# Performance work log

Hardware: AMD Instinct MI355X
Metric: run time of the kernel (lower is better)

The kernel has to match this reference:

```python
import jax, jax.numpy as jnp
import numpy as np

D_MODEL, H, KV, D = 2048, 32, 8, 64
G = H // KV  # groups = 4
B, T = 1, 2048


def rotate_half(x):
    # interleaved rotation: (-x1, x0, -x3, x2, ...)
    x_even = x[..., ::2]
    x_odd = x[..., 1::2]
    return jnp.stack((-x_odd, x_even), axis=-1).reshape(x.shape)


def setup_inputs() -> dict:
    key = jax.random.key(0)
    kx, kq, kk, kv, ko = jax.random.split(key, 5)
    x = jax.random.normal(kx, (B, T, D_MODEL), dtype=jnp.float32)
    # RoPE frequency table: freqs[0]=cos, freqs[1]=sin, each [T, D] with pairwise-repeated angles
    inv_freq = 1.0 / (10000.0 ** (jnp.arange(0, D, 2, dtype=jnp.float32) / D))  # [D/2]
    angles = jnp.arange(T, dtype=jnp.float32)[:, None] * inv_freq[None, :]       # [T, D/2]
    angles = jnp.repeat(angles, 2, axis=-1)                                       # [T, D]
    freqs = jnp.stack((jnp.cos(angles), jnp.sin(angles)), axis=0)                 # [2, T, D]
    # causal mask, broadcastable to [B, H, T, T]
    mask = jnp.tril(jnp.ones((T, T), dtype=bool))[None, None]
    s = 0.02
    Wq = s * jax.random.normal(kq, (D_MODEL, H * D), dtype=jnp.float32)
    Wk = s * jax.random.normal(kk, (D_MODEL, KV * D), dtype=jnp.float32)
    Wv = s * jax.random.normal(kv, (D_MODEL, KV * D), dtype=jnp.float32)
    Wo = s * jax.random.normal(ko, (D_MODEL, D_MODEL), dtype=jnp.float32)
    return {"x": x, "freqs": freqs, "mask": mask, "Wq": Wq, "Wk": Wk, "Wv": Wv, "Wo": Wo}


def reference(x, freqs, mask, Wq, Wk, Wv, Wo):
    b, t, _ = x.shape
    Q = (x @ Wq).reshape(b, t, H, D)
    K = (x @ Wk).reshape(b, t, KV, D)
    V = (x @ Wv).reshape(b, t, KV, D)
    cos = freqs[0, :t][None, :, None, :]  # [1,T,1,D]
    sin = freqs[1, :t][None, :, None, :]
    Q = Q * cos + rotate_half(Q) * sin
    K = K * cos + rotate_half(K) * sin
    # GQA: repeat each KV head `groups` times along the head axis
    K = jnp.repeat(K, G, axis=2)  # [B,T,H,D]
    V = jnp.repeat(V, G, axis=2)
    scale = D ** -0.5
    scores = jnp.einsum('bqhd,bkhd->bhqk', Q, K) * scale  # [B,H,T,T]
    scores = jnp.where(mask, scores, -jnp.inf)
    attn = jax.nn.softmax(scores, axis=-1)  # dropout=0.0 (eval) -> identity
    out = jnp.einsum('bhqk,bkhd->bqhd', attn, V).reshape(b, t, H * D)
    return out @ Wo
```

## Files before the change

kernel.cpp:

```cpp
#include <hip/hip_runtime.h>
#include <hip/hip_bf16.h>

#define T_SEQ  2048
#define DMODEL 2048
#define NH     32
#define NKV    8
#define HD     64

typedef __attribute__((ext_vector_type(8))) short bf16x8;
typedef __attribute__((ext_vector_type(4))) short bf16x4;
typedef __attribute__((ext_vector_type(4))) float f32x4;

__device__ __forceinline__ unsigned short f2bf(float f) {
    unsigned int u = __float_as_uint(f);
    return (unsigned short)((u + 0x7FFFu + ((u >> 16) & 1u)) >> 16);
}
__device__ __forceinline__ float bf2f(unsigned short b) {
    return __uint_as_float(((unsigned int)b) << 16);
}
__device__ __forceinline__ unsigned int pk2bf(float a, float b) {
    float2 f; f.x = a; f.y = b;
    __hip_bfloat162 h = __float22bfloat162_rn(f);
    union { __hip_bfloat162 h; unsigned int u; } cv; cv.h = h;
    return cv.u;
}
__device__ __forceinline__ int is_bf16(const void* __restrict__ freqs) {
    return ((const unsigned int*)freqs)[0] != 0x3F800000u;
}
__device__ __forceinline__ float ldf(const void* __restrict__ p, size_t i, int bf) {
    return bf ? bf2f(((const unsigned short*)p)[i]) : ((const float*)p)[i];
}

__global__ __launch_bounds__(256) void prep_kernel(const void* __restrict__ x,
                                                   const void* __restrict__ Wq,
                                                   const void* __restrict__ Wk,
                                                   const void* __restrict__ Wv,
                                                   unsigned short* __restrict__ xb,
                                                   unsigned short* __restrict__ WqT,
                                                   unsigned short* __restrict__ WkT,
                                                   unsigned short* __restrict__ WvT,
                                                   const void* __restrict__ freqs) {
    const int bf = is_bf16(freqs);
    const int t  = threadIdx.x;
    const int z  = blockIdx.z;
    if (z == 3) {
        const int r0 = blockIdx.y * 64, c0 = blockIdx.x * 64;
#pragma unroll
        for (int it = 0; it < 16; ++it) {
            int e = t + it * 256;
            size_t idx = (size_t)(r0 + (e >> 6)) * DMODEL + c0 + (e & 63);
            xb[idx] = bf ? ((const unsigned short*)x)[idx] : f2bf(((const float*)x)[idx]);
        }
        return;
    }
    const void* W; unsigned short* Wt; int N;
    if (z == 0)      { W = Wq; Wt = WqT; N = 2048; }
    else if (z == 1) { if (blockIdx.x >= 8) return; W = Wk; Wt = WkT; N = 512; }
    else             { if (blockIdx.x >= 8) return; W = Wv; Wt = WvT; N = 512; }
    __shared__ unsigned short Tl[64][65];
    const int n0 = blockIdx.x * 64, k0 = blockIdx.y * 64;
#pragma unroll
    for (int it = 0; it < 16; ++it) {
        int e = t + it * 256;
        int r = e >> 6, c = e & 63;
        Tl[r][c] = bf ? ((const unsigned short*)W)[(size_t)(k0 + r) * N + n0 + c]
                      : f2bf(((const float*)W)[(size_t)(k0 + r) * N + n0 + c]);
    }
    __syncthreads();
#pragma unroll
    for (int it = 0; it < 16; ++it) {
        int e = t + it * 256;
        int r = e >> 6, c = e & 63;
        Wt[(size_t)(n0 + r) * DMODEL + k0 + c] = Tl[c][r];
    }
}

__global__ __launch_bounds__(256) void trans_one(const void* __restrict__ W,
                                                 unsigned short* __restrict__ Wt,
                                                 const void* __restrict__ freqs) {
    const int bf = is_bf16(freqs);
    __shared__ unsigned short Tl[64][65];
    const int t = threadIdx.x;
    const int n0 = blockIdx.x * 64, k0 = blockIdx.y * 64;
#pragma unroll
    for (int it = 0; it < 16; ++it) {
        int e = t + it * 256;
        int r = e >> 6, c = e & 63;
        Tl[r][c] = bf ? ((const unsigned short*)W)[(size_t)(k0 + r) * DMODEL + n0 + c]
                      : f2bf(((const float*)W)[(size_t)(k0 + r) * DMODEL + n0 + c]);
    }
    __syncthreads();
#pragma unroll
    for (int it = 0; it < 16; ++it) {
        int e = t + it * 256;
        int r = e >> 6, c = e & 63;
        Wt[(size_t)(n0 + r) * DMODEL + k0 + c] = Tl[c][r];
    }
}

template <int WM, int WN, int CMODE>
__global__ __launch_bounds__(256) void gemm_mfma(const unsigned short* __restrict__ A,
                                                 const unsigned short* __restrict__ Bt,
                                                 void* __restrict__ C,
                                                 int M, int N, int K,
                                                 const void* __restrict__ freqs) {
    constexpr int BM  = 32 * WM;
    constexpr int BN  = 32 * WN;
    constexpr int LDT = 40;
    __shared__ unsigned short As[2][BM * LDT];
    __shared__ unsigned short Bs[2][BN * LDT];

    const int t    = threadIdx.x;
    const int w    = t >> 6;
    const int lane = t & 63;
    const int wm   = w & 1, wn = w >> 1;
    const int m0   = wm * WM * 16;
    const int n0   = wn * WN * 16;
    const int lrow = lane & 15;
    const int quad = lane >> 4;
    const int bm   = blockIdx.y * BM;
    const int bn   = blockIdx.x * BN;
    int cbf = 0;
    if (CMODE == 2) cbf = is_bf16(freqs);

    constexpr int AIT = (BM * 4) / 256;
    constexpr int BIT = (BN * 4) / 256;
    bf16x8 apre[AIT], bpre[BIT];

#pragma unroll
    for (int it = 0; it < AIT; ++it) {
        int c = t + it * 256;
        apre[it] = *(const bf16x8*)&A[(size_t)(bm + (c >> 2)) * K + (c & 3) * 8];
    }
#pragma unroll
    for (int it = 0; it < BIT; ++it) {
        int c = t + it * 256;
        bpre[it] = *(const bf16x8*)&Bt[(size_t)(bn + (c >> 2)) * K + (c & 3) * 8];
    }
#pragma unroll
    for (int it = 0; it < AIT; ++it) {
        int c = t + it * 256;
        *(bf16x8*)&As[0][(c >> 2) * LDT + (c & 3) * 8] = apre[it];
    }
#pragma unroll
    for (int it = 0; it < BIT; ++it) {
        int c = t + it * 256;
        *(bf16x8*)&Bs[0][(c >> 2) * LDT + (c & 3) * 8] = bpre[it];
    }

    f32x4 acc[WM][WN];
#pragma unroll
    for (int i = 0; i < WM; ++i)
#pragma unroll
        for (int j = 0; j < WN; ++j) acc[i][j] = (f32x4){0.f, 0.f, 0.f, 0.f};

    const int nk = K >> 5;
    for (int ki = 0; ki < nk; ++ki) {
        __syncthreads();
        const int buf = ki & 1;
        const bool pre = (ki + 1 < nk);
        if (pre) {
            const int k0 = (ki + 1) * 32;
#pragma unroll
            for (int it = 0; it < AIT; ++it) {
                int c = t + it * 256;
                apre[it] = *(const bf16x8*)&A[(size_t)(bm + (c >> 2)) * K + k0 + (c & 3) * 8];
            }
#pragma unroll
            for (int it = 0; it < BIT; ++it) {
                int c = t + it * 256;
                bpre[it] = *(const bf16x8*)&Bt[(size_t)(bn + (c >> 2)) * K + k0 + (c & 3) * 8];
            }
        }

        bf16x8 af[WM], bfr[WN];
#pragma unroll
        for (int i = 0; i < WM; ++i)
            af[i] = *(const bf16x8*)&As[buf][(m0 + i * 16 + lrow) * LDT + quad * 8];
#pragma unroll
        for (int j = 0; j < WN; ++j)
            bfr[j] = *(const bf16x8*)&Bs[buf][(n0 + j * 16 + lrow) * LDT + quad * 8];
#pragma unroll
        for (int i = 0; i < WM; ++i)
#pragma unroll
            for (int j = 0; j < WN; ++j)
                acc[i][j] = __builtin_amdgcn_mfma_f32_16x16x32_bf16(af[i], bfr[j], acc[i][j], 0, 0, 0);

        if (pre) {
#pragma unroll
            for (int it = 0; it < AIT; ++it) {
                int c = t + it * 256;
                *(bf16x8*)&As[buf ^ 1][(c >> 2) * LDT + (c & 3) * 8] = apre[it];
            }
#pragma unroll
            for (int it = 0; it < BIT; ++it) {
                int c = t + it * 256;
                *(bf16x8*)&Bs[buf ^ 1][(c >> 2) * LDT + (c & 3) * 8] = bpre[it];
            }
        }
    }

#pragma unroll
    for (int i = 0; i < WM; ++i)
#pragma unroll
        for (int j = 0; j < WN; ++j)
#pragma unroll
            for (int r = 0; r < 4; ++r) {
                int row = bm + m0 + i * 16 + quad * 4 + r;
                int col = bn + n0 + j * 16 + lrow;
                size_t idx = (size_t)row * N + col;
                float v = acc[i][j][r];
                if (CMODE == 1) ((unsigned short*)C)[idx] = f2bf(v);
                else { if (cbf) ((unsigned short*)C)[idx] = f2bf(v); else ((float*)C)[idx] = v; }
            }
}

__global__ __launch_bounds__(256) void kv_gemm(const unsigned short* __restrict__ A,
                                               const unsigned short* __restrict__ WkT,
                                               const unsigned short* __restrict__ WvT,
                                               unsigned short* __restrict__ Kb,
                                               unsigned short* __restrict__ Vt_g) {
    constexpr int LDT = 40;
    __shared__ unsigned short As[2][64 * LDT];
    __shared__ unsigned short Bs[2][64 * LDT];

    const int zv   = blockIdx.z;
    const unsigned short* Bt = zv ? WvT : WkT;
    const int t    = threadIdx.x;
    const int w    = t >> 6;
    const int lane = t & 63;
    const int wm   = w & 1, wn = w >> 1;
    const int m0   = wm * 32;
    const int n0   = wn * 32;
    const int lrow = lane & 15;
    const int quad = lane >> 4;
    const int bm   = blockIdx.y * 64;
    const int bn   = blockIdx.x * 64;
    const int K    = DMODEL, N = NKV * HD;

    bf16x8 apre, bpre;
    apre = *(const bf16x8*)&A[(size_t)(bm + (t >> 2)) * K + (t & 3) * 8];
    bpre = *(const bf16x8*)&Bt[(size_t)(bn + (t >> 2)) * K + (t & 3) * 8];
    *(bf16x8*)&As[0][(t >> 2) * LDT + (t & 3) * 8] = apre;
    *(bf16x8*)&Bs[0][(t >> 2) * LDT + (t & 3) * 8] = bpre;

    f32x4 acc[2][2];
#pragma unroll
    for (int i = 0; i < 2; ++i)
#pragma unroll
        for (int j = 0; j < 2; ++j) acc[i][j] = (f32x4){0.f, 0.f, 0.f, 0.f};

    const int nk = K >> 5;
    for (int ki = 0; ki < nk; ++ki) {
        __syncthreads();
        const int buf = ki & 1;
        const bool pre = (ki + 1 < nk);
        if (pre) {
            const int k0 = (ki + 1) * 32;
            apre = *(const bf16x8*)&A[(size_t)(bm + (t >> 2)) * K + k0 + (t & 3) * 8];
            bpre = *(const bf16x8*)&Bt[(size_t)(bn + (t >> 2)) * K + k0 + (t & 3) * 8];
        }
        bf16x8 af[2], bfr[2];
#pragma unroll
        for (int i = 0; i < 2; ++i)
            af[i] = *(const bf16x8*)&As[buf][(m0 + i * 16 + lrow) * LDT + quad * 8];
#pragma unroll
        for (int j = 0; j < 2; ++j)
            bfr[j] = *(const bf16x8*)&Bs[buf][(n0 + j * 16 + lrow) * LDT + quad * 8];
#pragma unroll
        for (int i = 0; i < 2; ++i)
#pragma unroll
            for (int j = 0; j < 2; ++j)
                acc[i][j] = __builtin_amdgcn_mfma_f32_16x16x32_bf16(af[i], bfr[j], acc[i][j], 0, 0, 0);
        if (pre) {
            *(bf16x8*)&As[buf ^ 1][(t >> 2) * LDT + (t & 3) * 8] = apre;
            *(bf16x8*)&Bs[buf ^ 1][(t >> 2) * LDT + (t & 3) * 8] = bpre;
        }
    }

#pragma unroll
    for (int i = 0; i < 2; ++i)
#pragma unroll
        for (int j = 0; j < 2; ++j)
#pragma unroll
            for (int r = 0; r < 4; ++r) {
                int row = bm + m0 + i * 16 + quad * 4 + r;
                int col = bn + n0 + j * 16 + lrow;
                unsigned short v = f2bf(acc[i][j][r]);
                if (zv) Vt_g[(size_t)col * T_SEQ + row] = v;
                else    Kb[(size_t)row * N + col] = v;
            }
}

__global__ void rope_kernel(unsigned short* __restrict__ Qb, unsigned short* __restrict__ Kb,
                            const void* __restrict__ freqs) {
    const int bf = is_bf16(freqs);
    int idx = blockIdx.x * blockDim.x + threadIdx.x;
    const int nq = T_SEQ * NH * 32;
    unsigned short* X; int nh; float scale; int li;
    if (idx < nq) { X = Qb; nh = NH; scale = 0.125f; li = idx; }
    else          { X = Kb; nh = NKV; scale = 1.0f; li = idx - nq;
                    if (li >= T_SEQ * NKV * 32) return; }
    int i = li & 31;
    int h = (li >> 5) % nh;
    int t = li / (nh * 32);
    float c = ldf(freqs, (size_t)t * 64 + 2 * i, bf);
    float s = ldf(freqs, (size_t)T_SEQ * 64 + (size_t)t * 64 + 2 * i, bf);
    int base = (t * nh + h) * HD + 2 * i;
    float x0 = bf2f(X[base]), x1 = bf2f(X[base + 1]);
    X[base]     = f2bf((x0 * c - x1 * s) * scale);
    X[base + 1] = f2bf((x1 * c + x0 * s) * scale);
}

__global__ __launch_bounds__(256) void attn_kernel(const unsigned short* __restrict__ Qb,
                                                   const unsigned short* __restrict__ Kb,
                                                   const unsigned short* __restrict__ Vt_g,
                                                   unsigned short* __restrict__ AO,
                                                   unsigned short* __restrict__ arena,
                                                   float* __restrict__ lpart) {
    __shared__ unsigned short Kf[2][8 * 64 * 8];
    __shared__ unsigned short Vf[2][8 * 64 * 8];

    const int t    = threadIdx.x;
    const int w    = t >> 6;
    const int lane = t & 63;
    const int lrow = lane & 15;
    const int quad = lane >> 4;
    const int hp   = blockIdx.y;
    const int kvh  = hp >> 1;
    const int h0   = kvh * 4 + (hp & 1) * 2;
    const int bxr  = 71 - (int)blockIdx.x;

    int qt, j, s;
    if (bxr < 8)       { qt = bxr; j = 0; s = 1; }
    else if (bxr < 24) { qt = 8 + ((bxr - 8) >> 1); j = (bxr - 8) & 1; s = 2; }
    else               { int e = bxr - 24; qt = 16 + e / 3; j = e % 3; s = 3; }
    const int n    = qt + 1;
    const int base = n / s, rem = n % s;
    const int nch  = base + (j < rem ? 1 : 0);
    const int cs   = j * base + (j < rem ? j : rem);
    const int q0   = qt * 64;
    const int koff = cs * 64;
    const bool mask_last = (cs + nch - 1) == qt;

    bf16x8 q_frag[2][2];
#pragma unroll
    for (int hh = 0; hh < 2; ++hh) {
        const unsigned short* qp = Qb + (size_t)(q0 + w * 16 + lrow) * (NH * HD) + (h0 + hh) * HD;
        q_frag[hh][0] = *(const bf16x8*)&qp[quad * 8];
        q_frag[hh][1] = *(const bf16x8*)&qp[32 + quad * 8];
    }

    const int    krow = 16 * w + lrow;
    const size_t vrow = (size_t)(kvh * HD + 16 * w + lrow) * T_SEQ;

    union U8 { bf16x8 v; bf16x4 hh[2]; unsigned short s[8]; unsigned int u32[4]; };

    bf16x8 kpre[2];
    bf16x4 vpre[2][2];
#pragma unroll
    for (int i = 0; i < 2; ++i) {
        kpre[i] = *(const bf16x8*)&Kb[(size_t)(koff + krow) * (NKV * HD) + kvh * HD + i * 32 + quad * 8];
        vpre[i][0] = *(const bf16x4*)&Vt_g[vrow + koff + i * 32 + quad * 4];
        vpre[i][1] = *(const bf16x4*)&Vt_g[vrow + koff + i * 32 + 16 + quad * 4];
    }
#pragma unroll
    for (int i = 0; i < 2; ++i) {
        *(bf16x8*)&Kf[0][((2 * w + i) * 64 + lane) * 8] = kpre[i];
        U8 u; u.hh[0] = vpre[i][0]; u.hh[1] = vpre[i][1];
        *(bf16x8*)&Vf[0][((2 * w + i) * 64 + lane) * 8] = u.v;
    }

    float l_s[2] = {0.0f, 0.0f};
    f32x4 oacc[2][4];
#pragma unroll
    for (int hh = 0; hh < 2; ++hh)
#pragma unroll
        for (int nc = 0; nc < 4; ++nc) oacc[hh][nc] = (f32x4){0.f, 0.f, 0.f, 0.f};

    for (int c = 0; c < nch; ++c) {
        __syncthreads();
        const int buf = c & 1;
        const bool pre = (c + 1 < nch);
        if (pre) {
            const int kb2 = koff + (c + 1) * 64;
#pragma unroll
            for (int i = 0; i < 2; ++i) {
                kpre[i] = *(const bf16x8*)&Kb[(size_t)(kb2 + krow) * (NKV * HD) + kvh * HD + i * 32 + quad * 8];
                vpre[i][0] = *(const bf16x4*)&Vt_g[vrow + kb2 + i * 32 + quad * 4];
                vpre[i][1] = *(const bf16x4*)&Vt_g[vrow + kb2 + i * 32 + 16 + quad * 4];
            }
        }

        f32x4 sacc[2][4];
#pragma unroll
        for (int hh = 0; hh < 2; ++hh)
#pragma unroll
            for (int kc = 0; kc < 4; ++kc) sacc[hh][kc] = (f32x4){0.f, 0.f, 0.f, 0.f};
#pragma unroll
        for (int kh = 0; kh < 2; ++kh) {
#pragma unroll
            for (int kc = 0; kc < 4; ++kc) {
                bf16x8 kf = *(const bf16x8*)&Kf[buf][((kc * 2 + kh) * 64 + lane) * 8];
                sacc[0][kc] = __builtin_amdgcn_mfma_f32_16x16x32_bf16(kf, q_frag[0][kh], sacc[0][kc], 0, 0, 0);
                sacc[1][kc] = __builtin_amdgcn_mfma_f32_16x16x32_bf16(kf, q_frag[1][kh], sacc[1][kc], 0, 0, 0);
            }
        }

        if (c == nch - 1 && mask_last) {
            const int qrow  = q0 + w * 16 + lrow;
            const int kbase = koff + c * 64 + quad * 4;
#pragma unroll
            for (int kc = 0; kc < 4; ++kc)
#pragma unroll
                for (int r = 0; r < 4; ++r)
                    if (kbase + kc * 16 + r > qrow) { sacc[0][kc][r] = -INFINITY; sacc[1][kc][r] = -INFINITY; }
        }

        bf16x8 pf[2][2];
#pragma unroll
        for (int hh = 0; hh < 2; ++hh) {
            float rsum = 0.0f;
#pragma unroll
            for (int kc = 0; kc < 4; ++kc)
#pragma unroll
                for (int r = 0; r < 4; ++r) {
                    sacc[hh][kc][r] = __expf(sacc[hh][kc][r]);
                    rsum += sacc[hh][kc][r];
                }
            l_s[hh] += rsum;
#pragma unroll
            for (int kh = 0; kh < 2; ++kh) {
                U8 u;
                u.u32[0] = pk2bf(sacc[hh][2 * kh][0], sacc[hh][2 * kh][1]);
                u.u32[1] = pk2bf(sacc[hh][2 * kh][2], sacc[hh][2 * kh][3]);
                u.u32[2] = pk2bf(sacc[hh][2 * kh + 1][0], sacc[hh][2 * kh + 1][1]);
                u.u32[3] = pk2bf(sacc[hh][2 * kh + 1][2], sacc[hh][2 * kh + 1][3]);
                pf[hh][kh] = u.v;
            }
        }

#pragma unroll
        for (int kh = 0; kh < 2; ++kh) {
#pragma unroll
            for (int nc = 0; nc < 4; ++nc) {
                bf16x8 vu = *(const bf16x8*)&Vf[buf][((nc * 2 + kh) * 64 + lane) * 8];
                oacc[0][nc] = __builtin_amdgcn_mfma_f32_16x16x32_bf16(pf[0][kh], vu, oacc[0][nc], 0, 0, 0);
                oacc[1][nc] = __builtin_amdgcn_mfma_f32_16x16x32_bf16(pf[1][kh], vu, oacc[1][nc], 0, 0, 0);
            }
        }

        if (pre) {
#pragma unroll
            for (int i = 0; i < 2; ++i) {
                *(bf16x8*)&Kf[buf ^ 1][((2 * w + i) * 64 + lane) * 8] = kpre[i];
                U8 u; u.hh[0] = vpre[i][0]; u.hh[1] = vpre[i][1];
                *(bf16x8*)&Vf[buf ^ 1][((2 * w + i) * 64 + lane) * 8] = u.v;
            }
        }
    }

#pragma unroll
    for (int hh = 0; hh < 2; ++hh) {
        const int h = h0 + hh;
        float ls = l_s[hh];
        ls += __shfl_xor(ls, 16);
        ls += __shfl_xor(ls, 32);

        if (s == 1) {
            const float linv = 1.0f / ls;
            float l_o[4];
#pragma unroll
            for (int r = 0; r < 4; ++r)
                l_o[r] = __shfl(linv, (lane & 48) | (quad * 4 + r));
#pragma unroll
            for (int nc = 0; nc < 4; ++nc)
#pragma unroll
                for (int r = 0; r < 4; ++r) {
                    int row = q0 + w * 16 + quad * 4 + r;
                    AO[(size_t)row * (NH * HD) + h * HD + nc * 16 + lrow] = f2bf(oacc[hh][nc][r] * l_o[r]);
                }
        } else {
            if (quad == 0)
                lpart[(((size_t)h * 32 + qt) * 3 + j) * 64 + (w * 16 + lrow)] = ls;
            if (j == 0) {
#pragma unroll
                for (int nc = 0; nc < 4; ++nc)
#pragma unroll
                    for (int r = 0; r < 4; ++r) {
                        int row = q0 + w * 16 + quad * 4 + r;
                        AO[(size_t)row * (NH * HD) + h * HD + nc * 16 + lrow] = f2bf(oacc[hh][nc][r]);
                    }
            } else {
                const int slot = (qt < 16) ? (qt - 8) : (8 + (qt - 16) * 2 + (j - 1));
                unsigned short* ap = arena + ((size_t)h * 40 + slot) * 4096;
#pragma unroll
                for (int nc = 0; nc < 4; ++nc)
#pragma unroll
                    for (int r = 0; r < 4; ++r)
                        ap[(size_t)(w * 16 + quad * 4 + r) * 64 + nc * 16 + lrow] = f2bf(oacc[hh][nc][r]);
            }
        }
    }
}

__global__ __launch_bounds__(256) void combine_kernel(unsigned short* __restrict__ AO,
                                                      const unsigned short* __restrict__ arena,
                                                      const float* __restrict__ lpart) {
    int idx = blockIdx.x * 256 + threadIdx.x;
    int row1 = idx >> 11;
    int col  = idx & 2047;
    int qt   = 8 + (row1 >> 6);
    int r    = row1 & 63;
    int h    = col >> 6;
    int d    = col & 63;
    int s    = (qt < 16) ? 2 : 3;

    size_t aoidx = (size_t)(512 + row1) * 2048 + col;
    float o = bf2f(AO[aoidx]);
    float l = lpart[(((size_t)h * 32 + qt) * 3 + 0) * 64 + r];
#pragma unroll
    for (int j = 1; j < 3; ++j) {
        if (j >= s) break;
        int slot = (qt < 16) ? (qt - 8) : (8 + (qt - 16) * 2 + (j - 1));
        o += bf2f(arena[((size_t)h * 40 + slot) * 4096 + (size_t)r * 64 + d]);
        l += lpart[(((size_t)h * 32 + qt) * 3 + j) * 64 + r];
    }
    AO[aoidx] = f2bf(o / l);
}

extern "C" void kernel_launch(void* const* d_in, const int* in_sizes, int n_in,
                              void* d_out, int out_size, void* d_ws, size_t ws_size,
                              hipStream_t stream) {
    const void* x     = d_in[0];
    const void* freqs = d_in[1];
    const void* Wq = d_in[3];
    const void* Wk = d_in[4];
    const void* Wv = d_in[5];
    const void* Wo = d_in[6];

    char* ws = (char*)d_ws;
    unsigned short* Qb   = (unsigned short*)(ws);
    unsigned short* Kb   = (unsigned short*)(ws + (8u  << 20));
    unsigned short* Vt_g = (unsigned short*)(ws + (10u << 20));
    unsigned short* xb   = (unsigned short*)(ws + (12u << 20));
    unsigned short* WT   = (unsigned short*)(ws + (20u << 20));
    unsigned short* WkT  = (unsigned short*)(ws + (28u << 20));
    unsigned short* WvT  = (unsigned short*)(ws + (30u << 20) + (512u << 10));
    unsigned short* arena = (unsigned short*)(ws + (28u << 20));
    float*          lprt  = (float*)(ws + (38u << 20));
    unsigned short* AOb  = xb;

    prep_kernel<<<dim3(32, 32, 4), 256, 0, stream>>>(x, Wq, Wk, Wv, xb, WT, WkT, WvT, freqs);

    gemm_mfma<2, 4, 1><<<dim3(DMODEL / 128, T_SEQ / 64), 256, 0, stream>>>(
        xb, WT, Qb, T_SEQ, DMODEL, DMODEL, nullptr);

    kv_gemm<<<dim3((NKV * HD) / 64, T_SEQ / 64, 2), 256, 0, stream>>>(xb, WkT, WvT, Kb, Vt_g);

    rope_kernel<<<(T_SEQ * (NH + NKV) * 32) / 256, 256, 0, stream>>>(Qb, Kb, freqs);

    trans_one<<<dim3(32, 32), 256, 0, stream>>>(Wo, WT, freqs);

    attn_kernel<<<dim3(72, 16), 256, 0, stream>>>(Qb, Kb, Vt_g, AOb, arena, lprt);

    combine_kernel<<<(1536 * 2048) / 256, 256, 0, stream>>>(AOb, arena, lprt);

    gemm_mfma<2, 4, 2><<<dim3(DMODEL / 128, T_SEQ / 64), 256, 0, stream>>>(
        AOb, WT, d_out, T_SEQ, DMODEL, DMODEL, freqs);
}
```

Baseline: 297.8 us.

## Fuse Q/K/V projections into one GEMM with direct global-to-LDS swizzled loads

The Q and separate K/V GEMMs are merged into a single GEMM over a concatenated transposed weight matrix (N=3072). The epilogue routes each column to Q, K, or transposed V. The shared GEMM core now uses global_load_lds to copy tiles straight into LDS with an XOR-swizzled layout instead of staging them through registers with padded rows. This removes a kernel launch, reduces register pressure and load/store instructions, and avoids LDS bank conflicts without padding. The trade-off is more complex addressing and reliance on the async LDS-load path, whose synchronisation must be correct.

```diff
diff --git a/kernel.cpp b/kernel.cpp
--- a/kernel.cpp
+++ b/kernel.cpp
@@ -29,6 +29,12 @@
 }
 __device__ __forceinline__ float ldf(const void* __restrict__ p, size_t i, int bf) {
     return bf ? bf2f(((const unsigned short*)p)[i]) : ((const float*)p)[i];
+}
+
+__device__ __forceinline__ void gload_lds16(const void* g, void* l) {
+    __builtin_amdgcn_global_load_lds(
+        (const __attribute__((address_space(1))) void*)g,
+        (__attribute__((address_space(3))) void*)l, 16, 0, 0);
 }
 
 __global__ __launch_bounds__(256) void prep_kernel(const void* __restrict__ x,
@@ -98,17 +104,15 @@
     }
 }
 
-template <int WM, int WN, int CMODE>
-__global__ __launch_bounds__(256) void gemm_mfma(const unsigned short* __restrict__ A,
-                                                 const unsigned short* __restrict__ Bt,
-                                                 void* __restrict__ C,
-                                                 int M, int N, int K,
-                                                 const void* __restrict__ freqs) {
-    constexpr int BM  = 32 * WM;
-    constexpr int BN  = 32 * WN;
-    constexpr int LDT = 40;
-    __shared__ unsigned short As[2][BM * LDT];
-    __shared__ unsigned short Bs[2][BN * LDT];
+template <int WM, int WN>
+__device__ __forceinline__ void gemm_core(const unsigned short* __restrict__ A,
+                                          const unsigned short* __restrict__ Bt,
+                                          int K, int bm, int bn,
+                                          f32x4 (&acc)[WM][WN]) {
+    constexpr int BM = 32 * WM;
+    constexpr int BN = 32 * WN;
+    __shared__ unsigned short As[2 * BM * 32];
+    __shared__ unsigned short Bs[2 * BN * 32];
 
     const int t    = threadIdx.x;
     const int w    = t >> 6;
@@ -118,177 +122,111 @@
     const int n0   = wn * WN * 16;
     const int lrow = lane & 15;
     const int quad = lane >> 4;
-    const int bm   = blockIdx.y * BM;
-    const int bn   = blockIdx.x * BN;
-    int cbf = 0;
-    if (CMODE == 2) cbf = is_bf16(freqs);
-
-    constexpr int AIT = (BM * 4) / 256;
-    constexpr int BIT = (BN * 4) / 256;
-    bf16x8 apre[AIT], bpre[BIT];
-
-#pragma unroll
-    for (int it = 0; it < AIT; ++it) {
-        int c = t + it * 256;
-        apre[it] = *(const bf16x8*)&A[(size_t)(bm + (c >> 2)) * K + (c & 3) * 8];
-    }
-#pragma unroll
-    for (int it = 0; it < BIT; ++it) {
-        int c = t + it * 256;
-        bpre[it] = *(const bf16x8*)&Bt[(size_t)(bn + (c >> 2)) * K + (c & 3) * 8];
-    }
-#pragma unroll
-    for (int it = 0; it < AIT; ++it) {
-        int c = t + it * 256;
-        *(bf16x8*)&As[0][(c >> 2) * LDT + (c & 3) * 8] = apre[it];
-    }
-#pragma unroll
-    for (int it = 0; it < BIT; ++it) {
-        int c = t + it * 256;
-        *(bf16x8*)&Bs[0][(c >> 2) * LDT + (c & 3) * 8] = bpre[it];
-    }
-
-    f32x4 acc[WM][WN];
+
+    const int l3    = (lane & 7) ^ ((lane >> 3) & 7);
+    const int srow  = ((lane >> 3) << 1) | (l3 >> 2);
+    const int selem = (l3 & 3) << 3;
+    const int ps3   = (((lrow & 1) << 2) | quad) ^ ((lrow >> 1) & 7);
+
 #pragma unroll
     for (int i = 0; i < WM; ++i)
 #pragma unroll
         for (int j = 0; j < WN; ++j) acc[i][j] = (f32x4){0.f, 0.f, 0.f, 0.f};
+
+#pragma unroll
+    for (int it = 0; it < BM / 16; ++it)
+        gload_lds16(&A[(size_t)(bm + it * 16 + srow) * K + selem], &As[it * 512]);
+#pragma unroll
+    for (int it = 0; it < BN / 16; ++it)
+        gload_lds16(&Bt[(size_t)(bn + it * 16 + srow) * K + selem], &Bs[it * 512]);
+    __syncthreads();
 
     const int nk = K >> 5;
     for (int ki = 0; ki < nk; ++ki) {
-        __syncthreads();
         const int buf = ki & 1;
-        const bool pre = (ki + 1 < nk);
-        if (pre) {
+        if (ki + 1 < nk) {
             const int k0 = (ki + 1) * 32;
 #pragma unroll
-            for (int it = 0; it < AIT; ++it) {
-                int c = t + it * 256;
-                apre[it] = *(const bf16x8*)&A[(size_t)(bm + (c >> 2)) * K + k0 + (c & 3) * 8];
-            }
-#pragma unroll
-            for (int it = 0; it < BIT; ++it) {
-                int c = t + it * 256;
-                bpre[it] = *(const bf16x8*)&Bt[(size_t)(bn + (c >> 2)) * K + k0 + (c & 3) * 8];
-            }
-        }
-
+            for (int it = 0; it < BM / 16; ++it)
+                gload_lds16(&A[(size_t)(bm + it * 16 + srow) * K + k0 + selem],
+                            &As[(buf ^ 1) * (BM * 32) + it * 512]);
+#pragma unroll
+            for (int it = 0; it < BN / 16; ++it)
+                gload_lds16(&Bt[(size_t)(bn + it * 16 + srow) * K + k0 + selem],
+                            &Bs[(buf ^ 1) * (BN * 32) + it * 512]);
+        }
         bf16x8 af[WM], bfr[WN];
 #pragma unroll
-        for (int i = 0; i < WM; ++i)
-            af[i] = *(const bf16x8*)&As[buf][(m0 + i * 16 + lrow) * LDT + quad * 8];
-#pragma unroll
-        for (int j = 0; j < WN; ++j)
-            bfr[j] = *(const bf16x8*)&Bs[buf][(n0 + j * 16 + lrow) * LDT + quad * 8];
+        for (int i = 0; i < WM; ++i) {
+            const int row = m0 + i * 16 + lrow;
+            af[i] = *(const bf16x8*)&As[buf * (BM * 32) + (row >> 1) * 64 + ps3 * 8];
+        }
+#pragma unroll
+        for (int j = 0; j < WN; ++j) {
+            const int row = n0 + j * 16 + lrow;
+            bfr[j] = *(const bf16x8*)&Bs[buf * (BN * 32) + (row >> 1) * 64 + ps3 * 8];
+        }
 #pragma unroll
         for (int i = 0; i < WM; ++i)
 #pragma unroll
             for (int j = 0; j < WN; ++j)
                 acc[i][j] = __builtin_amdgcn_mfma_f32_16x16x32_bf16(af[i], bfr[j], acc[i][j], 0, 0, 0);
-
-        if (pre) {
-#pragma unroll
-            for (int it = 0; it < AIT; ++it) {
-                int c = t + it * 256;
-                *(bf16x8*)&As[buf ^ 1][(c >> 2) * LDT + (c & 3) * 8] = apre[it];
-            }
-#pragma unroll
-            for (int it = 0; it < BIT; ++it) {
-                int c = t + it * 256;
-                *(bf16x8*)&Bs[buf ^ 1][(c >> 2) * LDT + (c & 3) * 8] = bpre[it];
-            }
-        }
-    }
-
-#pragma unroll
-    for (int i = 0; i < WM; ++i)
-#pragma unroll
-        for (int j = 0; j < WN; ++j)
+        __syncthreads();
+    }
+}
+
+__global__ __launch_bounds__(256) void gemm_mfma(const unsigned short* __restrict__ A,
+                                                 const unsigned short* __restrict__ Bt,
+                                                 void* __restrict__ C,
+                                                 int N, int K,
+                                                 const void* __restrict__ freqs) {
+    f32x4 acc[2][4];
+    const int bm = blockIdx.y * 64, bn = blockIdx.x * 128;
+    gemm_core<2, 4>(A, Bt, K, bm, bn, acc);
+
+    const int t = threadIdx.x, w = t >> 6, lane = t & 63;
+    const int m0 = (w & 1) * 32, n0 = (w >> 1) * 64;
+    const int lrow = lane & 15, quad = lane >> 4;
+    const int cbf = is_bf16(freqs);
+#pragma unroll
+    for (int i = 0; i < 2; ++i)
+#pragma unroll
+        for (int j = 0; j < 4; ++j)
 #pragma unroll
             for (int r = 0; r < 4; ++r) {
                 int row = bm + m0 + i * 16 + quad * 4 + r;
                 int col = bn + n0 + j * 16 + lrow;
                 size_t idx = (size_t)row * N + col;
                 float v = acc[i][j][r];
-                if (CMODE == 1) ((unsigned short*)C)[idx] = f2bf(v);
-                else { if (cbf) ((unsigned short*)C)[idx] = f2bf(v); else ((float*)C)[idx] = v; }
-            }
-}
-
-__global__ __launch_bounds__(256) void kv_gemm(const unsigned short* __restrict__ A,
-                                               const unsigned short* __restrict__ WkT,
-                                               const unsigned short* __restrict__ WvT,
-                                               unsigned short* __restrict__ Kb,
-                                               unsigned short* __restrict__ Vt_g) {
-    constexpr int LDT = 40;
-    __shared__ unsigned short As[2][64 * LDT];
-    __shared__ unsigned short Bs[2][64 * LDT];
-
-    const int zv   = blockIdx.z;
-    const unsigned short* Bt = zv ? WvT : WkT;
-    const int t    = threadIdx.x;
-    const int w    = t >> 6;
-    const int lane = t & 63;
-    const int wm   = w & 1, wn = w >> 1;
-    const int m0   = wm * 32;
-    const int n0   = wn * 32;
-    const int lrow = lane & 15;
-    const int quad = lane >> 4;
-    const int bm   = blockIdx.y * 64;
-    const int bn   = blockIdx.x * 64;
-    const int K    = DMODEL, N = NKV * HD;
-
-    bf16x8 apre, bpre;
-    apre = *(const bf16x8*)&A[(size_t)(bm + (t >> 2)) * K + (t & 3) * 8];
-    bpre = *(const bf16x8*)&Bt[(size_t)(bn + (t >> 2)) * K + (t & 3) * 8];
-    *(bf16x8*)&As[0][(t >> 2) * LDT + (t & 3) * 8] = apre;
-    *(bf16x8*)&Bs[0][(t >> 2) * LDT + (t & 3) * 8] = bpre;
-
-    f32x4 acc[2][2];
+                if (cbf) ((unsigned short*)C)[idx] = f2bf(v);
+                else     ((float*)C)[idx] = v;
+            }
+}
+
+__global__ __launch_bounds__(256) void gemm_qkv(const unsigned short* __restrict__ A,
+                                                const unsigned short* __restrict__ Bt,
+                                                unsigned short* __restrict__ Qb,
+                                                unsigned short* __restrict__ Kb,
+                                                unsigned short* __restrict__ Vt_g) {
+    f32x4 acc[2][4];
+    const int bm = blockIdx.y * 64, bn = blockIdx.x * 128;
+    gemm_core<2, 4>(A, Bt, DMODEL, bm, bn, acc);
+
+    const int t = threadIdx.x, w = t >> 6, lane = t & 63;
+    const int m0 = (w & 1) * 32, n0 = (w >> 1) * 64;
+    const int lrow = lane & 15, quad = lane >> 4;
 #pragma unroll
     for (int i = 0; i < 2; ++i)
 #pragma unroll
-        for (int j = 0; j < 2; ++j) acc[i][j] = (f32x4){0.f, 0.f, 0.f, 0.f};
-
-    const int nk = K >> 5;
-    for (int ki = 0; ki < nk; ++ki) {
-        __syncthreads();
-        const int buf = ki & 1;
-        const bool pre = (ki + 1 < nk);
-        if (pre) {
-            const int k0 = (ki + 1) * 32;
-            apre = *(const bf16x8*)&A[(size_t)(bm + (t >> 2)) * K + k0 + (t & 3) * 8];
-            bpre = *(const bf16x8*)&Bt[(size_t)(bn + (t >> 2)) * K + k0 + (t & 3) * 8];
-        }
-        bf16x8 af[2], bfr[2];
-#pragma unroll
-        for (int i = 0; i < 2; ++i)
-            af[i] = *(const bf16x8*)&As[buf][(m0 + i * 16 + lrow) * LDT + quad * 8];
-#pragma unroll
-        for (int j = 0; j < 2; ++j)
-            bfr[j] = *(const bf16x8*)&Bs[buf][(n0 + j * 16 + lrow) * LDT + quad * 8];
-#pragma unroll
-        for (int i = 0; i < 2; ++i)
-#pragma unroll
-            for (int j = 0; j < 2; ++j)
-                acc[i][j] = __builtin_amdgcn_mfma_f32_16x16x32_bf16(af[i], bfr[j], acc[i][j], 0, 0, 0);
-        if (pre) {
-            *(bf16x8*)&As[buf ^ 1][(t >> 2) * LDT + (t & 3) * 8] = apre;
-            *(bf16x8*)&Bs[buf ^ 1][(t >> 2) * LDT + (t & 3) * 8] = bpre;
-        }
-    }
-
-#pragma unroll
-    for (int i = 0; i < 2; ++i)
-#pragma unroll
-        for (int j = 0; j < 2; ++j)
+        for (int j = 0; j < 4; ++j)
 #pragma unroll
             for (int r = 0; r < 4; ++r) {
                 int row = bm + m0 + i * 16 + quad * 4 + r;
                 int col = bn + n0 + j * 16 + lrow;
                 unsigned short v = f2bf(acc[i][j][r]);
-                if (zv) Vt_g[(size_t)col * T_SEQ + row] = v;
-                else    Kb[(size_t)row * N + col] = v;
+                if (col < 2048)      Qb[(size_t)row * 2048 + col] = v;
+                else if (col < 2560) Kb[(size_t)row * 512 + (col - 2048)] = v;
+                else                 Vt_g[(size_t)(col - 2560) * T_SEQ + row] = v;
             }
 }
 
@@ -544,28 +482,25 @@
     unsigned short* Kb   = (unsigned short*)(ws + (8u  << 20));
     unsigned short* Vt_g = (unsigned short*)(ws + (10u << 20));
     unsigned short* xb   = (unsigned short*)(ws + (12u << 20));
-    unsigned short* WT   = (unsigned short*)(ws + (20u << 20));
-    unsigned short* WkT  = (unsigned short*)(ws + (28u << 20));
-    unsigned short* WvT  = (unsigned short*)(ws + (30u << 20) + (512u << 10));
+    unsigned short* WT3  = (unsigned short*)(ws + (20u << 20));
+    unsigned short* WkT  = WT3 + (size_t)2048 * 2048;
+    unsigned short* WvT  = WT3 + (size_t)2560 * 2048;
     unsigned short* arena = (unsigned short*)(ws + (28u << 20));
     float*          lprt  = (float*)(ws + (38u << 20));
     unsigned short* AOb  = xb;
 
-    prep_kernel<<<dim3(32, 32, 4), 256, 0, stream>>>(x, Wq, Wk, Wv, xb, WT, WkT, WvT, freqs);
-
-    gemm_mfma<2, 4, 1><<<dim3(DMODEL / 128, T_SEQ / 64), 256, 0, stream>>>(
-        xb, WT, Qb, T_SEQ, DMODEL, DMODEL, nullptr);
-
-    kv_gemm<<<dim3((NKV * HD) / 64, T_SEQ / 64, 2), 256, 0, stream>>>(xb, WkT, WvT, Kb, Vt_g);
+    prep_kernel<<<dim3(32, 32, 4), 256, 0, stream>>>(x, Wq, Wk, Wv, xb, WT3, WkT, WvT, freqs);
+
+    gemm_qkv<<<dim3(3072 / 128, T_SEQ / 64), 256, 0, stream>>>(xb, WT3, Qb, Kb, Vt_g);
 
     rope_kernel<<<(T_SEQ * (NH + NKV) * 32) / 256, 256, 0, stream>>>(Qb, Kb, freqs);
 
-    trans_one<<<dim3(32, 32), 256, 0, stream>>>(Wo, WT, freqs);
+    trans_one<<<dim3(32, 32), 256, 0, stream>>>(Wo, WT3, freqs);
 
     attn_kernel<<<dim3(72, 16), 256, 0, stream>>>(Qb, Kb, Vt_g, AOb, arena, lprt);
 
     combine_kernel<<<(1536 * 2048) / 256, 256, 0, stream>>>(AOb, arena, lprt);
 
-    gemm_mfma<2, 4, 2><<<dim3(DMODEL / 128, T_SEQ / 64), 256, 0, stream>>>(
-        AOb, WT, d_out, T_SEQ, DMODEL, DMODEL, freqs);
-}
+    gemm_mfma<<<dim3(DMODEL / 128, T_SEQ / 64), 256, 0, stream>>>(
+        AOb, WT3, d_out, DMODEL, DMODEL, freqs);
+}
```

Result: slower. 353.1 us (+18.6%).
